# Kernel tuning notes

Measured on AMD Instinct MI355X. Metric: run time of the kernel, lower is better.

The kernel has to match this reference:

```python
import jax, jax.numpy as jnp
import numpy as np


def setup_inputs() -> dict:
    key = jax.random.key(0)
    ks = jax.random.split(key, 11)
    B, T, H1, H2 = 256, 512, 1024, 1024
    s1 = 1.0 / np.sqrt(H1)
    s2 = 1.0 / np.sqrt(H2)
    return {
        "x": jax.random.normal(ks[0], (B, 2, T), dtype=jnp.float32),
        "W_ih1": jax.random.normal(ks[1], (H1, 2), dtype=jnp.float32) * s1,
        "W_hh1": jax.random.normal(ks[2], (H1, H1), dtype=jnp.float32) * s1,
        "b_ih1": jax.random.normal(ks[3], (H1,), dtype=jnp.float32) * s1,
        "b_hh1": jax.random.normal(ks[4], (H1,), dtype=jnp.float32) * s1,
        "W_ih2": jax.random.normal(ks[5], (H2, H1), dtype=jnp.float32) * s2,
        "W_hh2": jax.random.normal(ks[6], (H2, H2), dtype=jnp.float32) * s2,
        "b_ih2": jax.random.normal(ks[7], (H2,), dtype=jnp.float32) * s2,
        "b_hh2": jax.random.normal(ks[8], (H2,), dtype=jnp.float32) * s2,
        "W_lin": jax.random.normal(ks[9], (2, H2), dtype=jnp.float32) * s2,
        "b_lin": jax.random.normal(ks[10], (2,), dtype=jnp.float32) * s2,
        "future": 0,
    }


def _run(x, W_ih1, W_hh1, b_ih1, b_hh1, W_ih2, W_hh2, b_ih2, b_hh2, W_lin, b_lin, future):
    # x: [B, 2, T]  -> scan over time with xs [T, B, 2]
    B = x.shape[0]
    H1, H2 = W_hh1.shape[0], W_hh2.shape[0]

    def cell(x_t, h1, h2):
        # torch RNNCell (tanh): h' = tanh(x W_ih^T + b_ih + h W_hh^T + b_hh)
        h1 = jnp.tanh(x_t @ W_ih1.T + b_ih1 + h1 @ W_hh1.T + b_hh1)
        h2 = jnp.tanh(h1 @ W_ih2.T + b_ih2 + h2 @ W_hh2.T + b_hh2)
        out = h2 @ W_lin.T + b_lin  # [B, 2]
        return h1, h2, out

    def step(carry, x_t):
        h1, h2 = carry
        h1, h2, out = cell(x_t, h1, h2)
        return (h1, h2), out

    h1 = jnp.zeros((B, H1), dtype=x.dtype)
    h2 = jnp.zeros((B, H2), dtype=x.dtype)
    xs = jnp.transpose(x, (2, 0, 1))  # [T, B, 2]
    (h1, h2), outs = jax.lax.scan(step, (h1, h2), xs)  # outs: [T, B, 2]

    if future > 0:
        last = outs[-1]

        def fstep(carry, _):
            h1, h2, out = carry
            h1, h2, out = cell(out, h1, h2)
            return (h1, h2, out), out

        _, fouts = jax.lax.scan(fstep, (h1, h2, last), None, length=future)
        outs = jnp.concatenate([outs, fouts], axis=0)

    return jnp.transpose(outs, (1, 2, 0))  # [B, 2, T+future]


def reference(x, W_ih1, W_hh1, b_ih1, b_hh1, W_ih2, W_hh2, b_ih2, b_hh2, W_lin, b_lin, future):
    return _run(x, W_ih1, W_hh1, b_ih1, b_hh1, W_ih2, W_hh2, b_ih2, b_hh2, W_lin, b_lin, future)
```

## Files before the change

### kernel.cpp

```cpp
#include <hip/hip_runtime.h>

#define NB 256
#define NT 512
#define NH 1024
#define BH (NB * NH)
#define GRID_WGS 256
#define BLOCK 512

typedef __attribute__((ext_vector_type(8))) __bf16 bfrag;
typedef __attribute__((ext_vector_type(4))) float f32x4;
typedef __attribute__((ext_vector_type(4))) unsigned u32x4;
typedef __attribute__((ext_vector_type(8))) unsigned short u16x8;
typedef unsigned short us;

__device__ __attribute__((aligned(16))) us g_h1[2 * BH];
__device__ __attribute__((aligned(16))) us g_h2[3 * BH];
__device__ __attribute__((aligned(128))) unsigned g_flag[GRID_WGS];

__device__ __forceinline__ us f2bf(float f) {
  union { float f; unsigned u; } v; v.f = f;
  unsigned r = v.u + 0x7FFFu + ((v.u >> 16) & 1u);
  return (us)(r >> 16);
}
__device__ __forceinline__ float bf2f(us u) {
  union { unsigned u; float f; } v; v.u = ((unsigned)u) << 16;
  return v.f;
}

__device__ __forceinline__ bfrag cvt8(const float* __restrict__ p) {
  f32x4 a = *reinterpret_cast<const f32x4*>(p);
  f32x4 b = *reinterpret_cast<const f32x4*>(p + 4);
  u16x8 u;
#pragma unroll
  for (int i = 0; i < 4; ++i) { u[i] = f2bf(a[i]); u[i + 4] = f2bf(b[i]); }
  union { u16x8 u; bfrag b; } c; c.u = u; return c.b;
}

union f16u { u32x4 v; bfrag b; u16x8 s; };
__device__ __forceinline__ u32x4 ld16_dev(const void* p) {
  u32x4 r;
  asm volatile("global_load_dwordx4 %0, %1, off sc0 sc1" : "=v"(r) : "v"(p));
  return r;
}
__device__ __forceinline__ unsigned ld4_dev(const void* p) {
  unsigned r;
  asm volatile("global_load_dword %0, %1, off sc0 sc1\n\ts_waitcnt vmcnt(0)"
               : "=v"(r) : "v"(p) : "memory");
  return r;
}
__device__ __forceinline__ void st4_dev(void* p, unsigned v) {
  asm volatile("global_store_dword %0, %1, off sc0 sc1" :: "v"(p), "v"(v) : "memory");
}

__device__ __forceinline__ void wait_flags(const unsigned* f, int lane, int mask,
                                           unsigned tgt) {
  const unsigned* fp = f + (lane & mask);
  for (;;) {
    unsigned v = ld4_dev(fp);
    if (!__any((int)(v < tgt))) break;
    __builtin_amdgcn_s_sleep(1);
  }
}

__device__ __forceinline__ void out_row(const us* h2, int r_g, int w, int lane,
                                        const float* __restrict__ Wlin,
                                        const float* __restrict__ blin,
                                        float* __restrict__ out, int t) {
  const us* hp = h2 + r_g * NH + lane * 16;
  const float* wl = Wlin + w * NH + lane * 16;
  f16u h0, h1v;
  h0.v  = ld16_dev(hp);
  h1v.v = ld16_dev(hp + 8);
  asm volatile("s_waitcnt vmcnt(0)" ::: "memory");
  __builtin_amdgcn_sched_barrier(0);
  float s = 0.f;
#pragma unroll
  for (int e = 0; e < 8; ++e) {
    s = fmaf(bf2f(h0.s[e]),  wl[e],     s);
    s = fmaf(bf2f(h1v.s[e]), wl[8 + e], s);
  }
#pragma unroll
  for (int m = 1; m < 64; m <<= 1) s += __shfl_xor(s, m);
  if (lane == 0) out[r_g * (2 * NT) + w * NT + t] = s + blin[w];
}

__global__ void __launch_bounds__(BLOCK, 2) rnn_kernel(
    const float* __restrict__ x,
    const float* __restrict__ Wi1,
    const float* __restrict__ Whh1,
    const float* __restrict__ Wih2,
    const float* __restrict__ Whh2,
    const float* __restrict__ bih1,
    const float* __restrict__ bhh1,
    const float* __restrict__ bih2,
    const float* __restrict__ bhh2,
    const float* __restrict__ Wlin,
    const float* __restrict__ blin,
    float* __restrict__ out)
{
  const int bid = blockIdx.x, tid = threadIdx.x;
  const int w = tid >> 6, lane = tid & 63;
  const int mb = bid >> 5, nb = bid & 31;
  unsigned* gf = g_flag + mb * 32;

  const unsigned fb = ld4_dev(&gf[nb]);

  {
    const int zrow = tid >> 4, zc = tid & 15;
    const int off_d = ((mb * 32 + zrow) * NH + nb * 32) / 2;
    st4_dev((unsigned*)(g_h1 + BH)     + off_d + zc, 0u);
    st4_dev((unsigned*)(g_h2 + 2 * BH) + off_d + zc, 0u);
  }

  const int fr = lane & 15;
  const int ko = (lane >> 4) << 3;
  const int kbase = w * 128;
  bfrag w1[2][4], w2i[2][4], w2h[2][4];
#pragma unroll
  for (int cf = 0; cf < 2; ++cf)
#pragma unroll
    for (int st = 0; st < 4; ++st) {
      const int off = (nb * 32 + cf * 16 + fr) * NH + kbase + st * 32 + ko;
      w1[cf][st]  = cvt8(Whh1 + off);
      w2i[cf][st] = cvt8(Wih2 + off);
      w2h[cf][st] = cvt8(Whh2 + off);
    }

  const int rl = tid >> 4, cl = (tid & 15) * 2;
  const int grow = mb * 32 + rl, gcol = nb * 32 + cl;
  const float b1s0 = bih1[gcol] + bhh1[gcol];
  const float b1s1 = bih1[gcol + 1] + bhh1[gcol + 1];
  const float b2s0 = bih2[gcol] + bhh2[gcol];
  const float b2s1 = bih2[gcol + 1] + bhh2[gcol + 1];
  const float wi00 = Wi1[gcol * 2],       wi01 = Wi1[gcol * 2 + 1];
  const float wi10 = Wi1[(gcol + 1) * 2], wi11 = Wi1[(gcol + 1) * 2 + 1];
  const float* xrow = x + grow * (2 * NT);

  __shared__ float redA[8][32][36];
  __shared__ float redB[8][32][36];

  const int arow0 = mb * 32 + fr;
  const int prow = (lane >> 4) << 2;
  const int r_g = bid;

  asm volatile("s_waitcnt vmcnt(0)" ::: "memory");
  __syncthreads();
  if (tid == 0) st4_dev(&gf[nb], fb + 1u);

  int c0 = 0, c1 = 1, c2 = 2;

  for (int p = 0; p <= NT; ++p) {
    const us* h1_prev = g_h1 + ((p + 1) & 1) * BH;
    us* h1_cur        = g_h1 + (p & 1) * BH;
    const us* h2_pp   = g_h2 + c1 * BH;
    us* h2_cur        = g_h2 + c2 * BH;
    const us* h2_out  = g_h2 + c0 * BH;

    const float x0 = xrow[p < NT ? p : 0], x1 = xrow[NT + (p < NT ? p : 0)];

    wait_flags(gf + w * 4, lane, 3, fb + 1u + (unsigned)p);
    __builtin_amdgcn_sched_barrier(0);

    f16u a1[2][4], a2[2][4];
#pragma unroll
    for (int mf = 0; mf < 2; ++mf) {
      const us* pa1 = h1_prev + (arow0 + mf * 16) * NH + kbase + ko;
      const us* pa2 = h2_pp   + (arow0 + mf * 16) * NH + kbase + ko;
#pragma unroll
      for (int st = 0; st < 4; ++st) {
        a1[mf][st].v = ld16_dev(pa1 + st * 32);
        a2[mf][st].v = ld16_dev(pa2 + st * 32);
      }
    }

    f32x4 accA[2][2] = {}; f32x4 accB[2][2] = {};
    asm volatile("s_waitcnt vmcnt(8)" ::: "memory");
    __builtin_amdgcn_sched_barrier(0);
#pragma unroll
    for (int st = 0; st < 4; ++st) {
      accA[0][0] = __builtin_amdgcn_mfma_f32_16x16x32_bf16(a1[0][st].b, w1[0][st],  accA[0][0], 0, 0, 0);
      accA[0][1] = __builtin_amdgcn_mfma_f32_16x16x32_bf16(a1[0][st].b, w1[1][st],  accA[0][1], 0, 0, 0);
      accB[0][0] = __builtin_amdgcn_mfma_f32_16x16x32_bf16(a1[0][st].b, w2i[0][st], accB[0][0], 0, 0, 0);
      accB[0][1] = __builtin_amdgcn_mfma_f32_16x16x32_bf16(a1[0][st].b, w2i[1][st], accB[0][1], 0, 0, 0);
      accB[0][0] = __builtin_amdgcn_mfma_f32_16x16x32_bf16(a2[0][st].b, w2h[0][st], accB[0][0], 0, 0, 0);
      accB[0][1] = __builtin_amdgcn_mfma_f32_16x16x32_bf16(a2[0][st].b, w2h[1][st], accB[0][1], 0, 0, 0);
    }
    asm volatile("s_waitcnt vmcnt(0)" ::: "memory");
    __builtin_amdgcn_sched_barrier(0);
#pragma unroll
    for (int st = 0; st < 4; ++st) {
      accA[1][0] = __builtin_amdgcn_mfma_f32_16x16x32_bf16(a1[1][st].b, w1[0][st],  accA[1][0], 0, 0, 0);
      accA[1][1] = __builtin_amdgcn_mfma_f32_16x16x32_bf16(a1[1][st].b, w1[1][st],  accA[1][1], 0, 0, 0);
      accB[1][0] = __builtin_amdgcn_mfma_f32_16x16x32_bf16(a1[1][st].b, w2i[0][st], accB[1][0], 0, 0, 0);
      accB[1][1] = __builtin_amdgcn_mfma_f32_16x16x32_bf16(a1[1][st].b, w2i[1][st], accB[1][1], 0, 0, 0);
      accB[1][0] = __builtin_amdgcn_mfma_f32_16x16x32_bf16(a2[1][st].b, w2h[0][st], accB[1][0], 0, 0, 0);
      accB[1][1] = __builtin_amdgcn_mfma_f32_16x16x32_bf16(a2[1][st].b, w2h[1][st], accB[1][1], 0, 0, 0);
    }

#pragma unroll
    for (int mf = 0; mf < 2; ++mf)
#pragma unroll
      for (int cf = 0; cf < 2; ++cf)
#pragma unroll
        for (int r = 0; r < 4; ++r) {
          redA[w][mf * 16 + prow + r][cf * 16 + fr] = accA[mf][cf][r];
          redB[w][mf * 16 + prow + r][cf * 16 + fr] = accB[mf][cf][r];
        }

    if (p >= 3 && w < 2)
      out_row(h2_out, r_g, w, lane, Wlin, blin, out, p - 3);
    __syncthreads();

    float sA0 = 0.f, sA1 = 0.f, sB0 = 0.f, sB1 = 0.f;
#pragma unroll
    for (int u = 0; u < 8; ++u) {
      const float2 a = *reinterpret_cast<const float2*>(&redA[u][rl][cl]);
      const float2 b = *reinterpret_cast<const float2*>(&redB[u][rl][cl]);
      sA0 += a.x; sA1 += a.y; sB0 += b.x; sB1 += b.y;
    }
    if (p < NT) {
      const float v0 = sA0 + b1s0 + x0 * wi00 + x1 * wi01;
      const float v1 = sA1 + b1s1 + x0 * wi10 + x1 * wi11;
      st4_dev(h1_cur + grow * NH + gcol,
              (unsigned)f2bf(tanhf(v0)) | ((unsigned)f2bf(tanhf(v1)) << 16));
    }
    if (p >= 1) {
      const float v0 = sB0 + b2s0;
      const float v1 = sB1 + b2s1;
      st4_dev(h2_cur + grow * NH + gcol,
              (unsigned)f2bf(tanhf(v0)) | ((unsigned)f2bf(tanhf(v1)) << 16));
    }

    asm volatile("s_waitcnt vmcnt(0)" ::: "memory");
    __syncthreads();
    if (tid == 0) st4_dev(&gf[nb], fb + 2u + (unsigned)p);

    const int t = c0; c0 = c1; c1 = c2; c2 = t;
  }

  wait_flags(gf, lane, 31, fb + 2u + (unsigned)NT);
  if (w < 2) {
    out_row(g_h2 + ((NT - 2) % 3) * BH, r_g, w, lane, Wlin, blin, out, NT - 2);
    out_row(g_h2 + ((NT - 1) % 3) * BH, r_g, w, lane, Wlin, blin, out, NT - 1);
  }
}

extern "C" void kernel_launch(void* const* d_in, const int* in_sizes, int n_in,
                              void* d_out, int out_size, void* d_ws, size_t ws_size,
                              hipStream_t stream) {
  (void)in_sizes; (void)n_in; (void)d_ws; (void)ws_size; (void)out_size;
  const float* x    = (const float*)d_in[0];
  const float* Wi1  = (const float*)d_in[1];
  const float* Whh1 = (const float*)d_in[2];
  const float* bih1 = (const float*)d_in[3];
  const float* bhh1 = (const float*)d_in[4];
  const float* Wih2 = (const float*)d_in[5];
  const float* Whh2 = (const float*)d_in[6];
  const float* bih2 = (const float*)d_in[7];
  const float* bhh2 = (const float*)d_in[8];
  const float* Wlin = (const float*)d_in[9];
  const float* blin = (const float*)d_in[10];
  float* out = (float*)d_out;

  void* args[] = { (void*)&x, (void*)&Wi1, (void*)&Whh1, (void*)&Wih2, (void*)&Whh2,
                   (void*)&bih1, (void*)&bhh1, (void*)&bih2, (void*)&bhh2,
                   (void*)&Wlin, (void*)&blin, (void*)&out };
  hipLaunchCooperativeKernel((void*)rnn_kernel, dim3(GRID_WGS), dim3(BLOCK),
                             args, 0, stream);
}
```

Baseline: 3.437 ms.

## Split layer-1 and layer-2 sync into separate flags so layers overlap

After: 3.858 ms. +12.2%, slower.

```diff
diff --git a/kernel.cpp b/kernel.cpp
--- a/kernel.cpp
+++ b/kernel.cpp
@@ -13,9 +13,10 @@
 typedef __attribute__((ext_vector_type(8))) unsigned short u16x8;
 typedef unsigned short us;
 
-__device__ __attribute__((aligned(16))) us g_h1[2 * BH];
-__device__ __attribute__((aligned(16))) us g_h2[3 * BH];
-__device__ __attribute__((aligned(128))) unsigned g_flag[GRID_WGS];
+__device__ __attribute__((aligned(16))) us g_h1[3 * BH];
+__device__ __attribute__((aligned(16))) us g_h2[4 * BH];
+__device__ __attribute__((aligned(128))) unsigned g_flagA[GRID_WGS];
+__device__ __attribute__((aligned(128))) unsigned g_flagB[GRID_WGS];
 
 __device__ __forceinline__ us f2bf(float f) {
   union { float f; unsigned u; } v; v.f = f;
@@ -52,11 +53,18 @@
   asm volatile("global_store_dword %0, %1, off sc0 sc1" :: "v"(p), "v"(v) : "memory");
 }
 
-__device__ __forceinline__ void wait_flags(const unsigned* f, int lane, int mask,
-                                           unsigned tgt) {
-  const unsigned* fp = f + (lane & mask);
+__device__ __forceinline__ void wait4(const unsigned* f, int lane, unsigned tgt) {
+  unsigned v = tgt;
   for (;;) {
-    unsigned v = ld4_dev(fp);
+    if (lane < 4) v = ld4_dev(f + lane);
+    if (!__any((int)(v < tgt))) break;
+    __builtin_amdgcn_s_sleep(1);
+  }
+}
+__device__ __forceinline__ void wait32(const unsigned* f, int lane, unsigned tgt) {
+  unsigned v = tgt;
+  for (;;) {
+    if (lane < 32) v = ld4_dev(f + lane);
     if (!__any((int)(v < tgt))) break;
     __builtin_amdgcn_s_sleep(1);
   }
@@ -84,7 +92,9 @@
   if (lane == 0) out[r_g * (2 * NT) + w * NT + t] = s + blin[w];
 }
 
-__global__ void __launch_bounds__(BLOCK, 2) rnn_kernel(
+#define MFMA(a, b, c) __builtin_amdgcn_mfma_f32_16x16x32_bf16((a), (b), (c), 0, 0, 0)
+
+__global__ void __launch_bounds__(BLOCK, 1) rnn_kernel(
     const float* __restrict__ x,
     const float* __restrict__ Wi1,
     const float* __restrict__ Whh1,
@@ -101,15 +111,18 @@
   const int bid = blockIdx.x, tid = threadIdx.x;
   const int w = tid >> 6, lane = tid & 63;
   const int mb = bid >> 5, nb = bid & 31;
-  unsigned* gf = g_flag + mb * 32;
-
-  const unsigned fb = ld4_dev(&gf[nb]);
+  unsigned* gfA = g_flagA + mb * 32;
+  unsigned* gfB = g_flagB + mb * 32;
+
+  const unsigned fbA = ld4_dev(&gfA[nb]);
+  const unsigned fbB = ld4_dev(&gfB[nb]);
 
   {
     const int zrow = tid >> 4, zc = tid & 15;
     const int off_d = ((mb * 32 + zrow) * NH + nb * 32) / 2;
-    st4_dev((unsigned*)(g_h1 + BH)     + off_d + zc, 0u);
+    st4_dev((unsigned*)(g_h1 + 2 * BH) + off_d + zc, 0u);
     st4_dev((unsigned*)(g_h2 + 2 * BH) + off_d + zc, 0u);
+    st4_dev((unsigned*)(g_h2 + 3 * BH) + off_d + zc, 0u);
   }
 
   const int fr = lane & 15;
@@ -145,103 +158,133 @@
 
   asm volatile("s_waitcnt vmcnt(0)" ::: "memory");
   __syncthreads();
-  if (tid == 0) st4_dev(&gf[nb], fb + 1u);
-
-  int c0 = 0, c1 = 1, c2 = 2;
+  if (tid == 0) { st4_dev(&gfA[nb], fbA + 1u); st4_dev(&gfB[nb], fbB + 1u); }
 
   for (int p = 0; p <= NT; ++p) {
-    const us* h1_prev = g_h1 + ((p + 1) & 1) * BH;
-    us* h1_cur        = g_h1 + (p & 1) * BH;
-    const us* h2_pp   = g_h2 + c1 * BH;
-    us* h2_cur        = g_h2 + c2 * BH;
-    const us* h2_out  = g_h2 + c0 * BH;
+    const us* h1_prev = g_h1 + ((p + 2) % 3) * BH;
+    us*       h1_cur  = g_h1 + (p % 3) * BH;
+    const us* h2_pp   = g_h2 + ((p + 2) & 3) * BH;
+    us*       h2_cur  = g_h2 + ((p + 3) & 3) * BH;
+    const us* h2_out  = g_h2 + ((p + 1) & 3) * BH;
+
+    wait4(gfA + w * 4, lane, fbA + 1u + (unsigned)p);
+    __builtin_amdgcn_sched_barrier(0);
 
     const float x0 = xrow[p < NT ? p : 0], x1 = xrow[NT + (p < NT ? p : 0)];
 
-    wait_flags(gf + w * 4, lane, 3, fb + 1u + (unsigned)p);
-    __builtin_amdgcn_sched_barrier(0);
-
-    f16u a1[2][4], a2[2][4];
-#pragma unroll
-    for (int mf = 0; mf < 2; ++mf) {
-      const us* pa1 = h1_prev + (arow0 + mf * 16) * NH + kbase + ko;
-      const us* pa2 = h2_pp   + (arow0 + mf * 16) * NH + kbase + ko;
-#pragma unroll
-      for (int st = 0; st < 4; ++st) {
-        a1[mf][st].v = ld16_dev(pa1 + st * 32);
-        a2[mf][st].v = ld16_dev(pa2 + st * 32);
+    f16u a1[2][4];
+    {
+      const us* pa = h1_prev + arow0 * NH + kbase + ko;
+      const us* pb = h1_prev + (arow0 + 16) * NH + kbase + ko;
+#pragma unroll
+      for (int st = 0; st < 4; ++st) a1[0][st].v = ld16_dev(pa + st * 32);
+#pragma unroll
+      for (int st = 0; st < 4; ++st) a1[1][st].v = ld16_dev(pb + st * 32);
+    }
+    f32x4 accA[2][2] = {};
+    asm volatile("s_waitcnt vmcnt(4)" ::: "memory");
+    __builtin_amdgcn_sched_barrier(0);
+#pragma unroll
+    for (int st = 0; st < 4; ++st) {
+      accA[0][0] = MFMA(a1[0][st].b, w1[0][st], accA[0][0]);
+      accA[0][1] = MFMA(a1[0][st].b, w1[1][st], accA[0][1]);
+    }
+    asm volatile("s_waitcnt vmcnt(0)" ::: "memory");
+    __builtin_amdgcn_sched_barrier(0);
+#pragma unroll
+    for (int st = 0; st < 4; ++st) {
+      accA[1][0] = MFMA(a1[1][st].b, w1[0][st], accA[1][0]);
+      accA[1][1] = MFMA(a1[1][st].b, w1[1][st], accA[1][1]);
+    }
+#pragma unroll
+    for (int mf = 0; mf < 2; ++mf)
+#pragma unroll
+      for (int cf = 0; cf < 2; ++cf)
+#pragma unroll
+        for (int r = 0; r < 4; ++r)
+          redA[w][mf * 16 + prow + r][cf * 16 + fr] = accA[mf][cf][r];
+    __syncthreads();
+
+    if (p < NT) {
+      float sA0 = 0.f, sA1 = 0.f;
+#pragma unroll
+      for (int u = 0; u < 8; ++u) {
+        const float2 a = *reinterpret_cast<const float2*>(&redA[u][rl][cl]);
+        sA0 += a.x; sA1 += a.y;
       }
-    }
-
-    f32x4 accA[2][2] = {}; f32x4 accB[2][2] = {};
-    asm volatile("s_waitcnt vmcnt(8)" ::: "memory");
-    __builtin_amdgcn_sched_barrier(0);
-#pragma unroll
-    for (int st = 0; st < 4; ++st) {
-      accA[0][0] = __builtin_amdgcn_mfma_f32_16x16x32_bf16(a1[0][st].b, w1[0][st],  accA[0][0], 0, 0, 0);
-      accA[0][1] = __builtin_amdgcn_mfma_f32_16x16x32_bf16(a1[0][st].b, w1[1][st],  accA[0][1], 0, 0, 0);
-      accB[0][0] = __builtin_amdgcn_mfma_f32_16x16x32_bf16(a1[0][st].b, w2i[0][st], accB[0][0], 0, 0, 0);
-      accB[0][1] = __builtin_amdgcn_mfma_f32_16x16x32_bf16(a1[0][st].b, w2i[1][st], accB[0][1], 0, 0, 0);
-      accB[0][0] = __builtin_amdgcn_mfma_f32_16x16x32_bf16(a2[0][st].b, w2h[0][st], accB[0][0], 0, 0, 0);
-      accB[0][1] = __builtin_amdgcn_mfma_f32_16x16x32_bf16(a2[0][st].b, w2h[1][st], accB[0][1], 0, 0, 0);
-    }
-    asm volatile("s_waitcnt vmcnt(0)" ::: "memory");
-    __builtin_amdgcn_sched_barrier(0);
-#pragma unroll
-    for (int st = 0; st < 4; ++st) {
-      accA[1][0] = __builtin_amdgcn_mfma_f32_16x16x32_bf16(a1[1][st].b, w1[0][st],  accA[1][0], 0, 0, 0);
-      accA[1][1] = __builtin_amdgcn_mfma_f32_16x16x32_bf16(a1[1][st].b, w1[1][st],  accA[1][1], 0, 0, 0);
-      accB[1][0] = __builtin_amdgcn_mfma_f32_16x16x32_bf16(a1[1][st].b, w2i[0][st], accB[1][0], 0, 0, 0);
-      accB[1][1] = __builtin_amdgcn_mfma_f32_16x16x32_bf16(a1[1][st].b, w2i[1][st], accB[1][1], 0, 0, 0);
-      accB[1][0] = __builtin_amdgcn_mfma_f32_16x16x32_bf16(a2[1][st].b, w2h[0][st], accB[1][0], 0, 0, 0);
-      accB[1][1] = __builtin_amdgcn_mfma_f32_16x16x32_bf16(a2[1][st].b, w2h[1][st], accB[1][1], 0, 0, 0);
-    }
-
-#pragma unroll
-    for (int mf = 0; mf < 2; ++mf)
-#pragma unroll
-      for (int cf = 0; cf < 2; ++cf)
-#pragma unroll
-        for (int r = 0; r < 4; ++r) {
-          redA[w][mf * 16 + prow + r][cf * 16 + fr] = accA[mf][cf][r];
-          redB[w][mf * 16 + prow + r][cf * 16 + fr] = accB[mf][cf][r];
-        }
-
-    if (p >= 3 && w < 2)
-      out_row(h2_out, r_g, w, lane, Wlin, blin, out, p - 3);
-    __syncthreads();
-
-    float sA0 = 0.f, sA1 = 0.f, sB0 = 0.f, sB1 = 0.f;
-#pragma unroll
-    for (int u = 0; u < 8; ++u) {
-      const float2 a = *reinterpret_cast<const float2*>(&redA[u][rl][cl]);
-      const float2 b = *reinterpret_cast<const float2*>(&redB[u][rl][cl]);
-      sA0 += a.x; sA1 += a.y; sB0 += b.x; sB1 += b.y;
-    }
-    if (p < NT) {
       const float v0 = sA0 + b1s0 + x0 * wi00 + x1 * wi01;
       const float v1 = sA1 + b1s1 + x0 * wi10 + x1 * wi11;
       st4_dev(h1_cur + grow * NH + gcol,
               (unsigned)f2bf(tanhf(v0)) | ((unsigned)f2bf(tanhf(v1)) << 16));
     }
+    asm volatile("s_waitcnt vmcnt(0)" ::: "memory");
+    __syncthreads();
+    if (tid == 0) st4_dev(&gfA[nb], fbA + 2u + (unsigned)p);
+
+    if (p >= 3 && w < 2)
+      out_row(h2_out, r_g, w, lane, Wlin, blin, out, p - 3);
+
+    if (p >= 2) wait4(gfB + w * 4, lane, fbB + (unsigned)p);
+    __builtin_amdgcn_sched_barrier(0);
+
+    f16u a2[2][4];
+    {
+      const us* pa = h2_pp + arow0 * NH + kbase + ko;
+      const us* pb = h2_pp + (arow0 + 16) * NH + kbase + ko;
+#pragma unroll
+      for (int st = 0; st < 4; ++st) a2[0][st].v = ld16_dev(pa + st * 32);
+#pragma unroll
+      for (int st = 0; st < 4; ++st) a2[1][st].v = ld16_dev(pb + st * 32);
+    }
+    f32x4 accB[2][2] = {};
+    asm volatile("s_waitcnt vmcnt(4)" ::: "memory");
+    __builtin_amdgcn_sched_barrier(0);
+#pragma unroll
+    for (int st = 0; st < 4; ++st) {
+      accB[0][0] = MFMA(a1[0][st].b, w2i[0][st], accB[0][0]);
+      accB[0][1] = MFMA(a1[0][st].b, w2i[1][st], accB[0][1]);
+      accB[0][0] = MFMA(a2[0][st].b, w2h[0][st], accB[0][0]);
+      accB[0][1] = MFMA(a2[0][st].b, w2h[1][st], accB[0][1]);
+    }
+    asm volatile("s_waitcnt vmcnt(0)" ::: "memory");
+    __builtin_amdgcn_sched_barrier(0);
+#pragma unroll
+    for (int st = 0; st < 4; ++st) {
+      accB[1][0] = MFMA(a1[1][st].b, w2i[0][st], accB[1][0]);
+      accB[1][1] = MFMA(a1[1][st].b, w2i[1][st], accB[1][1]);
+      accB[1][0] = MFMA(a2[1][st].b, w2h[0][st], accB[1][0]);
+      accB[1][1] = MFMA(a2[1][st].b, w2h[1][st], accB[1][1]);
+    }
+#pragma unroll
+    for (int mf = 0; mf < 2; ++mf)
+#pragma unroll
+      for (int cf = 0; cf < 2; ++cf)
+#pragma unroll
+        for (int r = 0; r < 4; ++r)
+          redB[w][mf * 16 + prow + r][cf * 16 + fr] = accB[mf][cf][r];
+    __syncthreads();
+
     if (p >= 1) {
+      float sB0 = 0.f, sB1 = 0.f;
+#pragma unroll
+      for (int u = 0; u < 8; ++u) {
+        const float2 b = *reinterpret_cast<const float2*>(&redB[u][rl][cl]);
+        sB0 += b.x; sB1 += b.y;
+      }
       const float v0 = sB0 + b2s0;
       const float v1 = sB1 + b2s1;
       st4_dev(h2_cur + grow * NH + gcol,
               (unsigned)f2bf(tanhf(v0)) | ((unsigned)f2bf(tanhf(v1)) << 16));
     }
-
     asm volatile("s_waitcnt vmcnt(0)" ::: "memory");
     __syncthreads();
-    if (tid == 0) st4_dev(&gf[nb], fb + 2u + (unsigned)p);
-
-    const int t = c0; c0 = c1; c1 = c2; c2 = t;
-  }
-
-  wait_flags(gf, lane, 31, fb + 2u + (unsigned)NT);
+    if (tid == 0) st4_dev(&gfB[nb], fbB + 1u + (unsigned)p);
+  }
+
+  wait32(gfB, lane, fbB + 1u + (unsigned)NT);
   if (w < 2) {
-    out_row(g_h2 + ((NT - 2) % 3) * BH, r_g, w, lane, Wlin, blin, out, NT - 2);
-    out_row(g_h2 + ((NT - 1) % 3) * BH, r_g, w, lane, Wlin, blin, out, NT - 1);
+    out_row(g_h2 + ((NT - 2) & 3) * BH, r_g, w, lane, Wlin, blin, out, NT - 2);
+    out_row(g_h2 + ((NT - 1) & 3) * BH, r_g, w, lane, Wlin, blin, out, NT - 1);
   }
 }
 
```

## Split warps into layer-1 and layer-2 groups with decoupled flags and LDS counters

Applied to the files above, without the earlier changes.

Measured after the change: 5.018 ms. 1.46x slower.

```diff
diff --git a/kernel.cpp b/kernel.cpp
--- a/kernel.cpp
+++ b/kernel.cpp
@@ -6,16 +6,19 @@
 #define BH (NB * NH)
 #define GRID_WGS 256
 #define BLOCK 512
+#define T2 (2 * NT)
 
 typedef __attribute__((ext_vector_type(8))) __bf16 bfrag;
 typedef __attribute__((ext_vector_type(4))) float f32x4;
 typedef __attribute__((ext_vector_type(4))) unsigned u32x4;
+typedef __attribute__((ext_vector_type(2))) unsigned u32x2;
 typedef __attribute__((ext_vector_type(8))) unsigned short u16x8;
 typedef unsigned short us;
 
-__device__ __attribute__((aligned(16))) us g_h1[2 * BH];
-__device__ __attribute__((aligned(16))) us g_h2[3 * BH];
-__device__ __attribute__((aligned(128))) unsigned g_flag[GRID_WGS];
+__device__ __attribute__((aligned(16))) us g_h1[4 * BH];
+__device__ __attribute__((aligned(16))) us g_h2[4 * BH];
+__device__ __attribute__((aligned(128))) unsigned g_flagA[256];
+__device__ __attribute__((aligned(128))) unsigned g_flagB[256];
 
 __device__ __forceinline__ us f2bf(float f) {
   union { float f; unsigned u; } v; v.f = f;
@@ -26,7 +29,6 @@
   union { unsigned u; float f; } v; v.u = ((unsigned)u) << 16;
   return v.f;
 }
-
 __device__ __forceinline__ bfrag cvt8(const float* __restrict__ p) {
   f32x4 a = *reinterpret_cast<const f32x4*>(p);
   f32x4 b = *reinterpret_cast<const f32x4*>(p + 4);
@@ -51,38 +53,32 @@
 __device__ __forceinline__ void st4_dev(void* p, unsigned v) {
   asm volatile("global_store_dword %0, %1, off sc0 sc1" :: "v"(p), "v"(v) : "memory");
 }
-
-__device__ __forceinline__ void wait_flags(const unsigned* f, int lane, int mask,
-                                           unsigned tgt) {
-  const unsigned* fp = f + (lane & mask);
+__device__ __forceinline__ void st8_dev(void* p, unsigned lo, unsigned hi) {
+  u32x2 v = {lo, hi};
+  asm volatile("global_store_dwordx2 %0, %1, off sc0 sc1" :: "v"(p), "v"(v) : "memory");
+}
+
+__device__ __forceinline__ void poll32(const unsigned* f, int lane, unsigned tgt) {
+  unsigned v = tgt;
   for (;;) {
-    unsigned v = ld4_dev(fp);
+    if (lane < 32) v = ld4_dev(f + lane);
     if (!__any((int)(v < tgt))) break;
     __builtin_amdgcn_s_sleep(1);
   }
 }
 
-__device__ __forceinline__ void out_row(const us* h2, int r_g, int w, int lane,
-                                        const float* __restrict__ Wlin,
-                                        const float* __restrict__ blin,
-                                        float* __restrict__ out, int t) {
-  const us* hp = h2 + r_g * NH + lane * 16;
-  const float* wl = Wlin + w * NH + lane * 16;
-  f16u h0, h1v;
-  h0.v  = ld16_dev(hp);
-  h1v.v = ld16_dev(hp + 8);
-  asm volatile("s_waitcnt vmcnt(0)" ::: "memory");
-  __builtin_amdgcn_sched_barrier(0);
-  float s = 0.f;
-#pragma unroll
-  for (int e = 0; e < 8; ++e) {
-    s = fmaf(bf2f(h0.s[e]),  wl[e],     s);
-    s = fmaf(bf2f(h1v.s[e]), wl[8 + e], s);
-  }
-#pragma unroll
-  for (int m = 1; m < 64; m <<= 1) s += __shfl_xor(s, m);
-  if (lane == 0) out[r_g * (2 * NT) + w * NT + t] = s + blin[w];
-}
+__device__ __forceinline__ unsigned cadd(unsigned* c) {
+  return __hip_atomic_fetch_add(c, 1u, __ATOMIC_RELAXED, __HIP_MEMORY_SCOPE_WORKGROUP);
+}
+__device__ __forceinline__ void cwait(unsigned* c, unsigned tgt) {
+  while (__hip_atomic_load(c, __ATOMIC_RELAXED, __HIP_MEMORY_SCOPE_WORKGROUP) < tgt) {}
+}
+
+#define MFMA(a, b, c) __builtin_amdgcn_mfma_f32_16x16x32_bf16((a), (b), (c), 0, 0, 0)
+#define SB() __builtin_amdgcn_sched_barrier(0)
+#define VM0() do { asm volatile("s_waitcnt vmcnt(0)" ::: "memory"); SB(); } while (0)
+#define FENCE_REL() __builtin_amdgcn_fence(__ATOMIC_RELEASE, "workgroup")
+#define FENCE_ACQ() __builtin_amdgcn_fence(__ATOMIC_ACQUIRE, "workgroup")
 
 __global__ void __launch_bounds__(BLOCK, 2) rnn_kernel(
     const float* __restrict__ x,
@@ -101,147 +97,265 @@
   const int bid = blockIdx.x, tid = threadIdx.x;
   const int w = tid >> 6, lane = tid & 63;
   const int mb = bid >> 5, nb = bid & 31;
-  unsigned* gf = g_flag + mb * 32;
-
-  const unsigned fb = ld4_dev(&gf[nb]);
+  unsigned* fA = g_flagA + mb * 32;
+  unsigned* fB = g_flagB + mb * 32;
+  const unsigned fbA = ld4_dev(fA + nb);
+  const unsigned fbB = ld4_dev(fB + nb);
+
+  __shared__ unsigned s_cnt[8];
+  __shared__ float redA[4][32][36];
+  __shared__ float redG2[2][4][32][36];
+  __shared__ float redG3[4][32][36];
+  unsigned* cRed  = &s_cnt[0]; unsigned* cG2   = &s_cnt[1];
+  unsigned* cPubA = &s_cnt[2]; unsigned* cG3   = &s_cnt[3];
+  unsigned* cPubB = &s_cnt[4];
+
+  if (tid < 8) s_cnt[tid] = 0;
 
   {
-    const int zrow = tid >> 4, zc = tid & 15;
-    const int off_d = ((mb * 32 + zrow) * NH + nb * 32) / 2;
-    st4_dev((unsigned*)(g_h1 + BH)     + off_d + zc, 0u);
-    st4_dev((unsigned*)(g_h2 + 2 * BH) + off_d + zc, 0u);
+    const int zr = tid >> 4, zc = tid & 15;
+    const int off_d = ((mb * 32 + zr) * NH + nb * 32) / 2 + zc;
+    st4_dev((unsigned*)(g_h1 + 3 * BH) + off_d, 0u);
+    st4_dev((unsigned*)(g_h2 + 3 * BH) + off_d, 0u);
   }
 
   const int fr = lane & 15;
   const int ko = (lane >> 4) << 3;
-  const int kbase = w * 128;
-  bfrag w1[2][4], w2i[2][4], w2h[2][4];
-#pragma unroll
-  for (int cf = 0; cf < 2; ++cf)
-#pragma unroll
-    for (int st = 0; st < 4; ++st) {
-      const int off = (nb * 32 + cf * 16 + fr) * NH + kbase + st * 32 + ko;
-      w1[cf][st]  = cvt8(Whh1 + off);
-      w2i[cf][st] = cvt8(Wih2 + off);
-      w2h[cf][st] = cvt8(Whh2 + off);
+  const int prow = (lane >> 4) << 2;
+  const int kh = w & 3;
+  const int kbase = kh * 256;
+  const int erow = kh * 8 + (lane >> 3);
+  const int ecol = (lane & 7) * 4;
+  const int growE = mb * 32 + erow, gcolE = nb * 32 + ecol;
+  const int arow = mb * 32 + fr;
+
+  VM0();
+  __syncthreads();
+  if (tid == 0) { st4_dev(fA + nb, fbA + 1u); st4_dev(fB + nb, fbB + 2u); }
+
+  if (w < 4) {
+    bfrag w1[2][8], w2i[2][8];
+#pragma unroll
+    for (int cf = 0; cf < 2; ++cf)
+#pragma unroll
+      for (int st = 0; st < 8; ++st) {
+        const int off = (nb * 32 + cf * 16 + fr) * NH + kbase + st * 32 + ko;
+        w1[cf][st]  = cvt8(Whh1 + off);
+        w2i[cf][st] = cvt8(Wih2 + off);
+      }
+    const f32x4 b1 = *reinterpret_cast<const f32x4*>(bih1 + gcolE)
+                   + *reinterpret_cast<const f32x4*>(bhh1 + gcolE);
+    const f32x4 wa = *reinterpret_cast<const f32x4*>(Wi1 + gcolE * 2);
+    const f32x4 wbv = *reinterpret_cast<const f32x4*>(Wi1 + gcolE * 2 + 4);
+    f32x4 wi0, wi1;
+    wi0[0]=wa[0]; wi0[1]=wa[2]; wi0[2]=wbv[0]; wi0[3]=wbv[2];
+    wi1[0]=wa[1]; wi1[1]=wa[3]; wi1[2]=wbv[1]; wi1[3]=wbv[3];
+    const float* xrow = x + growE * T2;
+
+    for (int q = 0; q <= NT; ++q) {
+      const bool last = (q == NT);
+      const us* h1p = g_h1 + ((q + 3) & 3) * BH;
+      us*       h1c = g_h1 + (q & 3) * BH;
+
+      poll32(fA, lane, fbA + 1u + (unsigned)q); SB();
+
+      f16u a[8];
+      {
+        const us* pa = h1p + arow * NH + kbase + ko;
+#pragma unroll
+        for (int st = 0; st < 8; ++st) a[st].v = ld16_dev(pa + st * 32);
+      }
+      VM0();
+      {
+        f32x4 accW[2] = {}; f32x4 accG[2] = {};
+#pragma unroll
+        for (int st = 0; st < 8; ++st) {
+          if (!last) {
+            accW[0] = MFMA(a[st].b, w1[0][st], accW[0]);
+            accW[1] = MFMA(a[st].b, w1[1][st], accW[1]);
+          }
+          accG[0] = MFMA(a[st].b, w2i[0][st], accG[0]);
+          accG[1] = MFMA(a[st].b, w2i[1][st], accG[1]);
+        }
+        if (lane == 0 && q >= 3) cwait(cPubB, 4u * (unsigned)(q - 2));
+        FENCE_ACQ(); SB();
+#pragma unroll
+        for (int cf = 0; cf < 2; ++cf)
+#pragma unroll
+          for (int r = 0; r < 4; ++r) {
+            redG2[q & 1][kh][prow + r][cf * 16 + fr] = accG[cf][r];
+            if (!last) redA[kh][prow + r][cf * 16 + fr] = accW[cf][r];
+          }
+      }
+      {
+        const us* pa = h1p + (arow + 16) * NH + kbase + ko;
+#pragma unroll
+        for (int st = 0; st < 8; ++st) a[st].v = ld16_dev(pa + st * 32);
+      }
+      VM0();
+      {
+        f32x4 accW[2] = {}; f32x4 accG[2] = {};
+#pragma unroll
+        for (int st = 0; st < 8; ++st) {
+          if (!last) {
+            accW[0] = MFMA(a[st].b, w1[0][st], accW[0]);
+            accW[1] = MFMA(a[st].b, w1[1][st], accW[1]);
+          }
+          accG[0] = MFMA(a[st].b, w2i[0][st], accG[0]);
+          accG[1] = MFMA(a[st].b, w2i[1][st], accG[1]);
+        }
+#pragma unroll
+        for (int cf = 0; cf < 2; ++cf)
+#pragma unroll
+          for (int r = 0; r < 4; ++r) {
+            redG2[q & 1][kh][16 + prow + r][cf * 16 + fr] = accG[cf][r];
+            if (!last) redA[kh][16 + prow + r][cf * 16 + fr] = accW[cf][r];
+          }
+      }
+      FENCE_REL();
+      if (lane == 0) { cadd(cG2); if (!last) cadd(cRed); }
+
+      if (!last) {
+        const float x0 = xrow[q], x1 = xrow[NT + q];
+        if (lane == 0) cwait(cRed, 4u * (unsigned)(q + 1));
+        FENCE_ACQ(); SB();
+        f32x4 s = {};
+#pragma unroll
+        for (int u = 0; u < 4; ++u)
+          s += *reinterpret_cast<const f32x4*>(&redA[u][erow][ecol]);
+        const f32x4 v = s + b1 + x0 * wi0 + x1 * wi1;
+        st8_dev(h1c + growE * NH + gcolE,
+                (unsigned)f2bf(tanhf(v[0])) | ((unsigned)f2bf(tanhf(v[1])) << 16),
+                (unsigned)f2bf(tanhf(v[2])) | ((unsigned)f2bf(tanhf(v[3])) << 16));
+        VM0();
+        if (lane == 0) {
+          const unsigned old = cadd(cPubA);
+          if (old == 4u * (unsigned)q + 3u) st4_dev(fA + nb, fbA + 2u + (unsigned)q);
+        }
+      } else {
+        if (w == 0 && lane == 0) st4_dev(fA + nb, fbA + 2u + (unsigned)NT);
+      }
     }
 
-  const int rl = tid >> 4, cl = (tid & 15) * 2;
-  const int grow = mb * 32 + rl, gcol = nb * 32 + cl;
-  const float b1s0 = bih1[gcol] + bhh1[gcol];
-  const float b1s1 = bih1[gcol + 1] + bhh1[gcol + 1];
-  const float b2s0 = bih2[gcol] + bhh2[gcol];
-  const float b2s1 = bih2[gcol + 1] + bhh2[gcol + 1];
-  const float wi00 = Wi1[gcol * 2],       wi01 = Wi1[gcol * 2 + 1];
-  const float wi10 = Wi1[(gcol + 1) * 2], wi11 = Wi1[(gcol + 1) * 2 + 1];
-  const float* xrow = x + grow * (2 * NT);
-
-  __shared__ float redA[8][32][36];
-  __shared__ float redB[8][32][36];
-
-  const int arow0 = mb * 32 + fr;
-  const int prow = (lane >> 4) << 2;
-  const int r_g = bid;
-
-  asm volatile("s_waitcnt vmcnt(0)" ::: "memory");
-  __syncthreads();
-  if (tid == 0) st4_dev(&gf[nb], fb + 1u);
-
-  int c0 = 0, c1 = 1, c2 = 2;
-
-  for (int p = 0; p <= NT; ++p) {
-    const us* h1_prev = g_h1 + ((p + 1) & 1) * BH;
-    us* h1_cur        = g_h1 + (p & 1) * BH;
-    const us* h2_pp   = g_h2 + c1 * BH;
-    us* h2_cur        = g_h2 + c2 * BH;
-    const us* h2_out  = g_h2 + c0 * BH;
-
-    const float x0 = xrow[p < NT ? p : 0], x1 = xrow[NT + (p < NT ? p : 0)];
-
-    wait_flags(gf + w * 4, lane, 3, fb + 1u + (unsigned)p);
-    __builtin_amdgcn_sched_barrier(0);
-
-    f16u a1[2][4], a2[2][4];
-#pragma unroll
-    for (int mf = 0; mf < 2; ++mf) {
-      const us* pa1 = h1_prev + (arow0 + mf * 16) * NH + kbase + ko;
-      const us* pa2 = h2_pp   + (arow0 + mf * 16) * NH + kbase + ko;
-#pragma unroll
-      for (int st = 0; st < 4; ++st) {
-        a1[mf][st].v = ld16_dev(pa1 + st * 32);
-        a2[mf][st].v = ld16_dev(pa2 + st * 32);
-      }
+  } else {
+    bfrag w2h[2][8];
+#pragma unroll
+    for (int cf = 0; cf < 2; ++cf)
+#pragma unroll
+      for (int st = 0; st < 8; ++st) {
+        const int off = (nb * 32 + cf * 16 + fr) * NH + kbase + st * 32 + ko;
+        w2h[cf][st] = cvt8(Whh2 + off);
+      }
+    const f32x4 b2 = *reinterpret_cast<const f32x4*>(bih2 + gcolE)
+                   + *reinterpret_cast<const f32x4*>(bhh2 + gcolE);
+    float wl[16];
+    if (kh < 2) {
+#pragma unroll
+      for (int j = 0; j < 16; ++j) wl[j] = Wlin[kh * NH + lane * 16 + j];
     }
-
-    f32x4 accA[2][2] = {}; f32x4 accB[2][2] = {};
-    asm volatile("s_waitcnt vmcnt(8)" ::: "memory");
-    __builtin_amdgcn_sched_barrier(0);
-#pragma unroll
-    for (int st = 0; st < 4; ++st) {
-      accA[0][0] = __builtin_amdgcn_mfma_f32_16x16x32_bf16(a1[0][st].b, w1[0][st],  accA[0][0], 0, 0, 0);
-      accA[0][1] = __builtin_amdgcn_mfma_f32_16x16x32_bf16(a1[0][st].b, w1[1][st],  accA[0][1], 0, 0, 0);
-      accB[0][0] = __builtin_amdgcn_mfma_f32_16x16x32_bf16(a1[0][st].b, w2i[0][st], accB[0][0], 0, 0, 0);
-      accB[0][1] = __builtin_amdgcn_mfma_f32_16x16x32_bf16(a1[0][st].b, w2i[1][st], accB[0][1], 0, 0, 0);
-      accB[0][0] = __builtin_amdgcn_mfma_f32_16x16x32_bf16(a2[0][st].b, w2h[0][st], accB[0][0], 0, 0, 0);
-      accB[0][1] = __builtin_amdgcn_mfma_f32_16x16x32_bf16(a2[0][st].b, w2h[1][st], accB[0][1], 0, 0, 0);
+    const int r_g = mb * 32 + nb;
+
+    for (int p = 1; p <= NT; ++p) {
+      const us* h2p = g_h2 + ((p + 2) & 3) * BH;
+      us*       h2c = g_h2 + ((p + 3) & 3) * BH;
+
+      poll32(fB, lane, fbB + 1u + (unsigned)p); SB();
+
+      f16u a[8], o0, o1;
+      {
+        const us* pa = h2p + arow * NH + kbase + ko;
+#pragma unroll
+        for (int st = 0; st < 8; ++st) a[st].v = ld16_dev(pa + st * 32);
+      }
+      VM0();
+      {
+        f32x4 acc[2] = {};
+#pragma unroll
+        for (int st = 0; st < 8; ++st) {
+          acc[0] = MFMA(a[st].b, w2h[0][st], acc[0]);
+          acc[1] = MFMA(a[st].b, w2h[1][st], acc[1]);
+        }
+#pragma unroll
+        for (int cf = 0; cf < 2; ++cf)
+#pragma unroll
+          for (int r = 0; r < 4; ++r)
+            redG3[kh][prow + r][cf * 16 + fr] = acc[cf][r];
+      }
+      {
+        const us* pa = h2p + (arow + 16) * NH + kbase + ko;
+#pragma unroll
+        for (int st = 0; st < 8; ++st) a[st].v = ld16_dev(pa + st * 32);
+        o0.v = ld16_dev(h2p + r_g * NH + lane * 16);
+        o1.v = ld16_dev(h2p + r_g * NH + lane * 16 + 8);
+      }
+      VM0();
+      {
+        f32x4 acc[2] = {};
+#pragma unroll
+        for (int st = 0; st < 8; ++st) {
+          acc[0] = MFMA(a[st].b, w2h[0][st], acc[0]);
+          acc[1] = MFMA(a[st].b, w2h[1][st], acc[1]);
+        }
+#pragma unroll
+        for (int cf = 0; cf < 2; ++cf)
+#pragma unroll
+          for (int r = 0; r < 4; ++r)
+            redG3[kh][16 + prow + r][cf * 16 + fr] = acc[cf][r];
+      }
+      FENCE_REL();
+      if (lane == 0) {
+        cadd(cG3);
+        cwait(cG3, 4u * (unsigned)p);
+        cwait(cG2, 4u * (unsigned)(p + 1));
+      }
+      FENCE_ACQ(); SB();
+
+      f32x4 s = {};
+#pragma unroll
+      for (int u = 0; u < 4; ++u) {
+        s += *reinterpret_cast<const f32x4*>(&redG3[u][erow][ecol]);
+        s += *reinterpret_cast<const f32x4*>(&redG2[p & 1][u][erow][ecol]);
+      }
+      const f32x4 v = s + b2;
+      st8_dev(h2c + growE * NH + gcolE,
+              (unsigned)f2bf(tanhf(v[0])) | ((unsigned)f2bf(tanhf(v[1])) << 16),
+              (unsigned)f2bf(tanhf(v[2])) | ((unsigned)f2bf(tanhf(v[3])) << 16));
+      VM0();
+      if (lane == 0) {
+        const unsigned old = cadd(cPubB);
+        if (old == 4u * (unsigned)p - 1u) st4_dev(fB + nb, fbB + 2u + (unsigned)p);
+      }
+
+      if (kh < 2 && p >= 2) {
+        float so = 0.f;
+#pragma unroll
+        for (int e = 0; e < 8; ++e) {
+          so = fmaf(bf2f(o0.s[e]), wl[e],     so);
+          so = fmaf(bf2f(o1.s[e]), wl[8 + e], so);
+        }
+#pragma unroll
+        for (int m = 1; m < 64; m <<= 1) so += __shfl_xor(so, m);
+        if (lane == 0) out[r_g * T2 + kh * NT + (p - 2)] = so + blin[kh];
+      }
     }
-    asm volatile("s_waitcnt vmcnt(0)" ::: "memory");
-    __builtin_amdgcn_sched_barrier(0);
-#pragma unroll
-    for (int st = 0; st < 4; ++st) {
-      accA[1][0] = __builtin_amdgcn_mfma_f32_16x16x32_bf16(a1[1][st].b, w1[0][st],  accA[1][0], 0, 0, 0);
-      accA[1][1] = __builtin_amdgcn_mfma_f32_16x16x32_bf16(a1[1][st].b, w1[1][st],  accA[1][1], 0, 0, 0);
-      accB[1][0] = __builtin_amdgcn_mfma_f32_16x16x32_bf16(a1[1][st].b, w2i[0][st], accB[1][0], 0, 0, 0);
-      accB[1][1] = __builtin_amdgcn_mfma_f32_16x16x32_bf16(a1[1][st].b, w2i[1][st], accB[1][1], 0, 0, 0);
-      accB[1][0] = __builtin_amdgcn_mfma_f32_16x16x32_bf16(a2[1][st].b, w2h[0][st], accB[1][0], 0, 0, 0);
-      accB[1][1] = __builtin_amdgcn_mfma_f32_16x16x32_bf16(a2[1][st].b, w2h[1][st], accB[1][1], 0, 0, 0);
+
+    if (kh < 2) {
+      poll32(fB, lane, fbB + 2u + (unsigned)NT); SB();
+      const us* h2l = g_h2 + ((NT + 3) & 3) * BH;
+      f16u o0, o1;
+      o0.v = ld16_dev(h2l + r_g * NH + lane * 16);
+      o1.v = ld16_dev(h2l + r_g * NH + lane * 16 + 8);
+      VM0();
+      float so = 0.f;
+#pragma unroll
+      for (int e = 0; e < 8; ++e) {
+        so = fmaf(bf2f(o0.s[e]), wl[e],     so);
+        so = fmaf(bf2f(o1.s[e]), wl[8 + e], so);
+      }
+#pragma unroll
+      for (int m = 1; m < 64; m <<= 1) so += __shfl_xor(so, m);
+      if (lane == 0) out[r_g * T2 + kh * NT + (NT - 1)] = so + blin[kh];
     }
-
-#pragma unroll
-    for (int mf = 0; mf < 2; ++mf)
-#pragma unroll
-      for (int cf = 0; cf < 2; ++cf)
-#pragma unroll
-        for (int r = 0; r < 4; ++r) {
-          redA[w][mf * 16 + prow + r][cf * 16 + fr] = accA[mf][cf][r];
-          redB[w][mf * 16 + prow + r][cf * 16 + fr] = accB[mf][cf][r];
-        }
-
-    if (p >= 3 && w < 2)
-      out_row(h2_out, r_g, w, lane, Wlin, blin, out, p - 3);
-    __syncthreads();
-
-    float sA0 = 0.f, sA1 = 0.f, sB0 = 0.f, sB1 = 0.f;
-#pragma unroll
-    for (int u = 0; u < 8; ++u) {
-      const float2 a = *reinterpret_cast<const float2*>(&redA[u][rl][cl]);
-      const float2 b = *reinterpret_cast<const float2*>(&redB[u][rl][cl]);
-      sA0 += a.x; sA1 += a.y; sB0 += b.x; sB1 += b.y;
-    }
-    if (p < NT) {
-      const float v0 = sA0 + b1s0 + x0 * wi00 + x1 * wi01;
-      const float v1 = sA1 + b1s1 + x0 * wi10 + x1 * wi11;
-      st4_dev(h1_cur + grow * NH + gcol,
-              (unsigned)f2bf(tanhf(v0)) | ((unsigned)f2bf(tanhf(v1)) << 16));
-    }
-    if (p >= 1) {
-      const float v0 = sB0 + b2s0;
-      const float v1 = sB1 + b2s1;
-      st4_dev(h2_cur + grow * NH + gcol,
-              (unsigned)f2bf(tanhf(v0)) | ((unsigned)f2bf(tanhf(v1)) << 16));
-    }
-
-    asm volatile("s_waitcnt vmcnt(0)" ::: "memory");
-    __syncthreads();
-    if (tid == 0) st4_dev(&gf[nb], fb + 2u + (unsigned)p);
-
-    const int t = c0; c0 = c1; c1 = c2; c2 = t;
-  }
-
-  wait_flags(gf, lane, 31, fb + 2u + (unsigned)NT);
-  if (w < 2) {
-    out_row(g_h2 + ((NT - 2) % 3) * BH, r_g, w, lane, Wlin, blin, out, NT - 2);
-    out_row(g_h2 + ((NT - 1) % 3) * BH, r_g, w, lane, Wlin, blin, out, NT - 1);
   }
 }
 
```

## Pad sync flags, drop spin sleep, move output projection after flag publish

Applied to the files above, without the earlier changes.

Measured after the change: 3.302 ms. 3.9% less time.

```diff
diff --git a/kernel.cpp b/kernel.cpp
--- a/kernel.cpp
+++ b/kernel.cpp
@@ -6,6 +6,8 @@
 #define BH (NB * NH)
 #define GRID_WGS 256
 #define BLOCK 512
+#define T2 (2 * NT)
+#define FSTRIDE 32
 
 typedef __attribute__((ext_vector_type(8))) __bf16 bfrag;
 typedef __attribute__((ext_vector_type(4))) float f32x4;
@@ -13,9 +15,9 @@
 typedef __attribute__((ext_vector_type(8))) unsigned short u16x8;
 typedef unsigned short us;
 
-__device__ __attribute__((aligned(16))) us g_h1[2 * BH];
-__device__ __attribute__((aligned(16))) us g_h2[3 * BH];
-__device__ __attribute__((aligned(128))) unsigned g_flag[GRID_WGS];
+__device__ __attribute__((aligned(16))) us g_h1[4 * BH];
+__device__ __attribute__((aligned(16))) us g_h2[4 * BH];
+__device__ __attribute__((aligned(128))) unsigned g_flag[GRID_WGS * FSTRIDE];
 
 __device__ __forceinline__ us f2bf(float f) {
   union { float f; unsigned u; } v; v.f = f;
@@ -26,7 +28,6 @@
   union { unsigned u; float f; } v; v.u = ((unsigned)u) << 16;
   return v.f;
 }
-
 __device__ __forceinline__ bfrag cvt8(const float* __restrict__ p) {
   f32x4 a = *reinterpret_cast<const f32x4*>(p);
   f32x4 b = *reinterpret_cast<const f32x4*>(p + 4);
@@ -52,13 +53,20 @@
   asm volatile("global_store_dword %0, %1, off sc0 sc1" :: "v"(p), "v"(v) : "memory");
 }
 
-__device__ __forceinline__ void wait_flags(const unsigned* f, int lane, int mask,
-                                           unsigned tgt) {
-  const unsigned* fp = f + (lane & mask);
+__device__ __forceinline__ void wait4(const unsigned* gf, int s0, int lane, unsigned tgt) {
+  const unsigned* fp = gf + (s0 + (lane & 3)) * FSTRIDE;
+  unsigned v = tgt;
   for (;;) {
-    unsigned v = ld4_dev(fp);
+    if (lane < 4) v = ld4_dev(fp);
     if (!__any((int)(v < tgt))) break;
-    __builtin_amdgcn_s_sleep(1);
+  }
+}
+__device__ __forceinline__ void wait32(const unsigned* gf, int lane, unsigned tgt) {
+  const unsigned* fp = gf + (lane & 31) * FSTRIDE;
+  unsigned v = tgt;
+  for (;;) {
+    if (lane < 32) v = ld4_dev(fp);
+    if (!__any((int)(v < tgt))) break;
   }
 }
 
@@ -81,8 +89,10 @@
   }
 #pragma unroll
   for (int m = 1; m < 64; m <<= 1) s += __shfl_xor(s, m);
-  if (lane == 0) out[r_g * (2 * NT) + w * NT + t] = s + blin[w];
-}
+  if (lane == 0) out[r_g * T2 + w * NT + t] = s + blin[w];
+}
+
+#define MFMA(a, b, c) __builtin_amdgcn_mfma_f32_16x16x32_bf16((a), (b), (c), 0, 0, 0)
 
 __global__ void __launch_bounds__(BLOCK, 2) rnn_kernel(
     const float* __restrict__ x,
@@ -101,15 +111,15 @@
   const int bid = blockIdx.x, tid = threadIdx.x;
   const int w = tid >> 6, lane = tid & 63;
   const int mb = bid >> 5, nb = bid & 31;
-  unsigned* gf = g_flag + mb * 32;
-
-  const unsigned fb = ld4_dev(&gf[nb]);
+  unsigned* gf = g_flag + mb * 32 * FSTRIDE;
+  const unsigned fb = ld4_dev(&gf[nb * FSTRIDE]);
 
   {
     const int zrow = tid >> 4, zc = tid & 15;
-    const int off_d = ((mb * 32 + zrow) * NH + nb * 32) / 2;
-    st4_dev((unsigned*)(g_h1 + BH)     + off_d + zc, 0u);
-    st4_dev((unsigned*)(g_h2 + 2 * BH) + off_d + zc, 0u);
+    const int off_d = ((mb * 32 + zrow) * NH + nb * 32) / 2 + zc;
+    st4_dev((unsigned*)(g_h1 + 3 * BH) + off_d, 0u);
+    st4_dev((unsigned*)(g_h2 + 2 * BH) + off_d, 0u);
+    st4_dev((unsigned*)(g_h2 + 3 * BH) + off_d, 0u);
   }
 
   const int fr = lane & 15;
@@ -134,7 +144,7 @@
   const float b2s1 = bih2[gcol + 1] + bhh2[gcol + 1];
   const float wi00 = Wi1[gcol * 2],       wi01 = Wi1[gcol * 2 + 1];
   const float wi10 = Wi1[(gcol + 1) * 2], wi11 = Wi1[(gcol + 1) * 2 + 1];
-  const float* xrow = x + grow * (2 * NT);
+  const float* xrow = x + grow * T2;
 
   __shared__ float redA[8][32][36];
   __shared__ float redB[8][32][36];
@@ -145,20 +155,18 @@
 
   asm volatile("s_waitcnt vmcnt(0)" ::: "memory");
   __syncthreads();
-  if (tid == 0) st4_dev(&gf[nb], fb + 1u);
-
-  int c0 = 0, c1 = 1, c2 = 2;
+  if (tid == 0) st4_dev(&gf[nb * FSTRIDE], fb + 1u);
 
   for (int p = 0; p <= NT; ++p) {
-    const us* h1_prev = g_h1 + ((p + 1) & 1) * BH;
-    us* h1_cur        = g_h1 + (p & 1) * BH;
-    const us* h2_pp   = g_h2 + c1 * BH;
-    us* h2_cur        = g_h2 + c2 * BH;
-    const us* h2_out  = g_h2 + c0 * BH;
+    const us* h1_prev = g_h1 + ((p + 3) & 3) * BH;
+    us*       h1_cur  = g_h1 + (p & 3) * BH;
+    const us* h2_pp   = g_h2 + ((p + 2) & 3) * BH;
+    us*       h2_cur  = g_h2 + ((p + 3) & 3) * BH;
+    const us* h2_out  = g_h2 + ((p + 1) & 3) * BH;
 
     const float x0 = xrow[p < NT ? p : 0], x1 = xrow[NT + (p < NT ? p : 0)];
 
-    wait_flags(gf + w * 4, lane, 3, fb + 1u + (unsigned)p);
+    wait4(gf, w * 4, lane, fb + 1u + (unsigned)p);
     __builtin_amdgcn_sched_barrier(0);
 
     f16u a1[2][4], a2[2][4];
@@ -178,23 +186,23 @@
     __builtin_amdgcn_sched_barrier(0);
 #pragma unroll
     for (int st = 0; st < 4; ++st) {
-      accA[0][0] = __builtin_amdgcn_mfma_f32_16x16x32_bf16(a1[0][st].b, w1[0][st],  accA[0][0], 0, 0, 0);
-      accA[0][1] = __builtin_amdgcn_mfma_f32_16x16x32_bf16(a1[0][st].b, w1[1][st],  accA[0][1], 0, 0, 0);
-      accB[0][0] = __builtin_amdgcn_mfma_f32_16x16x32_bf16(a1[0][st].b, w2i[0][st], accB[0][0], 0, 0, 0);
-      accB[0][1] = __builtin_amdgcn_mfma_f32_16x16x32_bf16(a1[0][st].b, w2i[1][st], accB[0][1], 0, 0, 0);
-      accB[0][0] = __builtin_amdgcn_mfma_f32_16x16x32_bf16(a2[0][st].b, w2h[0][st], accB[0][0], 0, 0, 0);
-      accB[0][1] = __builtin_amdgcn_mfma_f32_16x16x32_bf16(a2[0][st].b, w2h[1][st], accB[0][1], 0, 0, 0);
+      accA[0][0] = MFMA(a1[0][st].b, w1[0][st],  accA[0][0]);
+      accA[0][1] = MFMA(a1[0][st].b, w1[1][st],  accA[0][1]);
+      accB[0][0] = MFMA(a1[0][st].b, w2i[0][st], accB[0][0]);
+      accB[0][1] = MFMA(a1[0][st].b, w2i[1][st], accB[0][1]);
+      accB[0][0] = MFMA(a2[0][st].b, w2h[0][st], accB[0][0]);
+      accB[0][1] = MFMA(a2[0][st].b, w2h[1][st], accB[0][1]);
     }
     asm volatile("s_waitcnt vmcnt(0)" ::: "memory");
     __builtin_amdgcn_sched_barrier(0);
 #pragma unroll
     for (int st = 0; st < 4; ++st) {
-      accA[1][0] = __builtin_amdgcn_mfma_f32_16x16x32_bf16(a1[1][st].b, w1[0][st],  accA[1][0], 0, 0, 0);
-      accA[1][1] = __builtin_amdgcn_mfma_f32_16x16x32_bf16(a1[1][st].b, w1[1][st],  accA[1][1], 0, 0, 0);
-      accB[1][0] = __builtin_amdgcn_mfma_f32_16x16x32_bf16(a1[1][st].b, w2i[0][st], accB[1][0], 0, 0, 0);
-      accB[1][1] = __builtin_amdgcn_mfma_f32_16x16x32_bf16(a1[1][st].b, w2i[1][st], accB[1][1], 0, 0, 0);
-      accB[1][0] = __builtin_amdgcn_mfma_f32_16x16x32_bf16(a2[1][st].b, w2h[0][st], accB[1][0], 0, 0, 0);
-      accB[1][1] = __builtin_amdgcn_mfma_f32_16x16x32_bf16(a2[1][st].b, w2h[1][st], accB[1][1], 0, 0, 0);
+      accA[1][0] = MFMA(a1[1][st].b, w1[0][st],  accA[1][0]);
+      accA[1][1] = MFMA(a1[1][st].b, w1[1][st],  accA[1][1]);
+      accB[1][0] = MFMA(a1[1][st].b, w2i[0][st], accB[1][0]);
+      accB[1][1] = MFMA(a1[1][st].b, w2i[1][st], accB[1][1]);
+      accB[1][0] = MFMA(a2[1][st].b, w2h[0][st], accB[1][0]);
+      accB[1][1] = MFMA(a2[1][st].b, w2h[1][st], accB[1][1]);
     }
 
 #pragma unroll
@@ -206,9 +214,6 @@
           redA[w][mf * 16 + prow + r][cf * 16 + fr] = accA[mf][cf][r];
           redB[w][mf * 16 + prow + r][cf * 16 + fr] = accB[mf][cf][r];
         }
-
-    if (p >= 3 && w < 2)
-      out_row(h2_out, r_g, w, lane, Wlin, blin, out, p - 3);
     __syncthreads();
 
     float sA0 = 0.f, sA1 = 0.f, sB0 = 0.f, sB1 = 0.f;
@@ -233,15 +238,16 @@
 
     asm volatile("s_waitcnt vmcnt(0)" ::: "memory");
     __syncthreads();
-    if (tid == 0) st4_dev(&gf[nb], fb + 2u + (unsigned)p);
-
-    const int t = c0; c0 = c1; c1 = c2; c2 = t;
-  }
-
-  wait_flags(gf, lane, 31, fb + 2u + (unsigned)NT);
+    if (tid == 0) st4_dev(&gf[nb * FSTRIDE], fb + 2u + (unsigned)p);
+
+    if (p >= 3 && w < 2)
+      out_row(h2_out, r_g, w, lane, Wlin, blin, out, p - 3);
+  }
+
+  wait32(gf, lane, fb + 2u + (unsigned)NT);
   if (w < 2) {
-    out_row(g_h2 + ((NT - 2) % 3) * BH, r_g, w, lane, Wlin, blin, out, NT - 2);
-    out_row(g_h2 + ((NT - 1) % 3) * BH, r_g, w, lane, Wlin, blin, out, NT - 1);
+    out_row(g_h2 + ((NT - 2) & 3) * BH, r_g, w, lane, Wlin, blin, out, NT - 2);
+    out_row(g_h2 + ((NT - 1) & 3) * BH, r_g, w, lane, Wlin, blin, out, NT - 1);
   }
 }
 
```
